# Performance work log

Hardware: AMD Instinct MI355X
Metric: run time of the kernel (lower is better)

Reference implementation:

```python
import jax, jax.numpy as jnp
import numpy as np

CONF_THRES = 0.6   # non_max_suppression default
IOU_THRES = 0.45   # non_max_suppression default
MAX_WH = 4096.0    # class-offset trick constant
MAX_DET = 300
NC = 80


def xywh2xyxy(b):
    xy, wh = b[:, :2], b[:, 2:4]
    return jnp.concatenate([xy - wh / 2, xy + wh / 2], axis=1)


def box_iou(a, b):
    # a: [N,4], b: [M,4] xyxy -> [N,M]
    area_a = (a[:, 2] - a[:, 0]) * (a[:, 3] - a[:, 1])
    area_b = (b[:, 2] - b[:, 0]) * (b[:, 3] - b[:, 1])
    lt = jnp.maximum(a[:, None, :2], b[None, :, :2])
    rb = jnp.minimum(a[:, None, 2:], b[None, :, 2:])
    wh = jnp.clip(rb - lt, 0.0)
    inter = wh[..., 0] * wh[..., 1]
    return inter / (area_a[:, None] + area_b[None, :] - inter + 1e-9)


def nms_image(x):
    # x: [N, 85] = [xywh, obj, 80 class logits]
    N = x.shape[0]
    logits = x[:, 5:]
    obj = x[:, 4]
    cls = logits * obj[:, None]          # x[:,5:] *= x[:,4:5]
    box = xywh2xyxy(x[:, :4])
    conf = cls.max(axis=1)
    j = jnp.argmax(cls, axis=1)
    valid = (obj > CONF_THRES) & (conf > CONF_THRES)
    scores = jnp.where(valid, conf, -1.0)  # invalid sort last, never suppress
    boxes_off = box + (j.astype(x.dtype) * MAX_WH)[:, None]  # class offset NMS

    order = jnp.argsort(-scores)
    iou = box_iou(boxes_off[order], boxes_off[order])  # [N,N]
    idxs = jnp.arange(N)

    def body(i, keep):
        sup = (iou[i] > IOU_THRES) & (idxs > i) & keep[i]
        return keep & ~sup

    keep = jax.lax.fori_loop(0, N, body, valid[order])

    # rows = [xyxy, conf, cls_idx, 80 logits] in score-sorted order
    rows = jnp.concatenate([
        box[order],
        conf[order][:, None],
        j[order].astype(x.dtype)[:, None],
        logits[order],
    ], axis=1)  # [N, 86]

    rank = jnp.cumsum(keep) - 1
    dest = jnp.where(keep & (rank < MAX_DET), rank, MAX_DET)  # dropped -> slot MAX_DET
    out = jnp.zeros((MAX_DET + 1, rows.shape[1]), x.dtype).at[dest].set(rows)
    return out[:MAX_DET]  # [300, 86]; zero rows = no detection


def setup_inputs() -> dict:
    key = jax.random.key(0)
    score = jax.random.normal(key, (32, 425, 17, 17), dtype=jnp.float32)
    return {"score": score}


def reference(score):
    B, C, H, W = score.shape
    # view(B, 425, H*W).transpose(1,2).view(B, H*W*5, 85)
    pred = score.reshape(B, C, H * W)
    pred = jnp.transpose(pred, (0, 2, 1)).reshape(B, H * W * 5, 85)
    return jax.vmap(nms_image)(pred)  # [B, 300, 86] = [xyxy, conf, cls, 80 logits]
```

## Files before the change

### kernel.cpp

```cpp
#include <hip/hip_runtime.h>

#define NPRED 1445
#define RAWSTR 1472
#define NCLS  80
#define MAXDET 300
#define OUTC  86
#define CONF_T 0.6f
#define IOU_T  0.45f
#define MAX_WH 4096.0f
#define HWSZ  289
#define NIMG  32
#define SLOTS 768
#define MCAP  512
#define EPB   256
#define EWALK 2048

#define OFF_CNT  128
#define OFF_KEYR 256
#define OFF_BOXR 377088
#define OFF_KEY  1130752
#define OFF_SBOX 1327360
#define OFF_ECNT 1720576
#define OFF_EDG  1721600
#define OFF_DST  1983744
#define WS_NEED  2022144

__device__ __forceinline__ unsigned long long bcast64(unsigned long long v, int srcLane) {
    unsigned lo = (unsigned)__builtin_amdgcn_readlane((int)(unsigned)(v & 0xFFFFFFFFULL), srcLane);
    unsigned hi = (unsigned)__builtin_amdgcn_readlane((int)(unsigned)(v >> 32), srcLane);
    return ((unsigned long long)hi << 32) | lo;
}

__global__ __launch_bounds__(128)
void prep_kernel(const float* __restrict__ score, unsigned long long* __restrict__ wsKeyRaw,
                 float4* __restrict__ wsBoxRaw) {
    const int b = blockIdx.x;
    const int ci = blockIdx.y * 128 + threadIdx.x;
    if (ci >= NPRED) return;
    const int t5 = ci / HWSZ;
    const int hw = ci - t5 * HWSZ;
    const int n = hw * 5 + t5;
    const float* base = score + (size_t)b * 425 * HWSZ + (size_t)(t5 * 85) * HWSZ + hw;
    float x = base[0];
    float y = base[HWSZ];
    float w = base[2 * HWSZ];
    float h = base[3 * HWSZ];
    float obj = base[4 * HWSZ];

    float best = -INFINITY; int bj = 0;
    #pragma unroll 16
    for (int k = 0; k < NCLS; ++k) {
        float v = base[(5 + k) * HWSZ] * obj;
        if (v > best) { best = v; bj = k; }
    }

    float wh2 = w * 0.5f, hh2 = h * 0.5f;
    float x1 = x - wh2, y1 = y - hh2, x2 = x + wh2, y2 = y + hh2;
    float off = (float)bj * MAX_WH;

    unsigned long long key = ~0ULL;
    if ((obj > CONF_T) && (best > CONF_T)) {
        unsigned int u = __float_as_uint(best);
        unsigned int desc = ~(u | 0x80000000u);
        key = ((unsigned long long)desc << 32)
            | ((unsigned long long)(unsigned)n << 16)
            | ((unsigned long long)(unsigned)bj << 8);
    }
    wsKeyRaw[b * RAWSTR + ci] = key;
    wsBoxRaw[b * RAWSTR + ci] = make_float4(x1 + off, y1 + off, x2 + off, y2 + off);
}

struct EdgeSh {
    unsigned long long keys[NPRED];
    unsigned long long cke[SLOTS];
    unsigned short cidx[SLOTS];
    float sx1[SLOTS], sy1[SLOTS], sx2[SLOTS], sy2[SLOTS];
    int wtot[16];
    int mTot, ecnt;
};

__global__ __launch_bounds__(1024)
void edge_kernel(const unsigned long long* __restrict__ wsKeyRaw,
                 const float4* __restrict__ wsBoxRaw,
                 int* __restrict__ wsCnt, unsigned long long* __restrict__ wsKey,
                 float4* __restrict__ wsSBox,
                 int* __restrict__ wsECnt, unsigned int* __restrict__ wsEdges) {
    __shared__ EdgeSh s;
    const int b = blockIdx.x, w = blockIdx.y, tid = threadIdx.x;
    const int lane = tid & 63, wid = tid >> 6;

    for (int i = tid; i < NPRED; i += 1024) s.keys[i] = wsKeyRaw[b * RAWSTR + i];
    if (tid == 0) s.ecnt = 0;
    __syncthreads();

    const int i0 = tid, i1 = tid + 1024;
    const bool v0 = (s.keys[i0] >> 63) == 0ULL;
    const bool v1 = (i1 < NPRED) && ((s.keys[i1] >> 63) == 0ULL);
    int cnt = (int)v0 + (int)v1;
    int inc = cnt;
    #pragma unroll
    for (int m = 1; m < 64; m <<= 1) {
        int v = __shfl_up(inc, m, 64);
        if (lane >= m) inc += v;
    }
    if (lane == 63) s.wtot[wid] = inc;
    __syncthreads();
    int basep = 0;
    for (int w2 = 0; w2 < wid; ++w2) basep += s.wtot[w2];
    int pos = basep + inc - cnt;
    if (v0 && pos < SLOTS) s.cidx[pos] = (unsigned short)i0;
    if (v1 && pos + (int)v0 < SLOTS) s.cidx[pos + (int)v0] = (unsigned short)i1;
    if (tid == 0) {
        int t = 0;
        for (int w2 = 0; w2 < 16; ++w2) t += s.wtot[w2];
        s.mTot = t;
    }
    __syncthreads();
    int M = s.mTot; if (M > SLOTS) M = SLOTS;
    if (tid < M) s.cke[tid] = s.keys[s.cidx[tid]];
    __syncthreads();

    if (tid < M) {
        unsigned long long ki = s.cke[tid];
        int rank = 0;
        #pragma unroll 4
        for (int j2 = 0; j2 < M; ++j2) rank += (s.cke[j2] < ki) ? 1 : 0;
        float4 bx = wsBoxRaw[b * RAWSTR + s.cidx[tid]];
        s.sx1[rank] = bx.x; s.sy1[rank] = bx.y; s.sx2[rank] = bx.z; s.sy2[rank] = bx.w;
        if (w == 0) {
            wsKey[b * SLOTS + rank] = ki;
            wsSBox[b * SLOTS + rank] = bx;
        }
    }
    if (w == 0 && tid == 0) wsCnt[b] = M;
    __syncthreads();

    if (M > MCAP) { if (tid == 0) wsECnt[b * 8 + w] = 0x7FFFFFFF; return; }

    unsigned int* reg = wsEdges + (size_t)(b * 8 + w) * EPB;
    const int j = (w << 6) + lane;
    float jx1 = 0.f, jy1 = 0.f, jx2 = 0.f, jy2 = 0.f, ab = 0.f;
    const bool jok = (j < M);
    if (jok) {
        jx1 = s.sx1[j]; jy1 = s.sy1[j]; jx2 = s.sx2[j]; jy2 = s.sy2[j];
        ab = (jx2 - jx1) * (jy2 - jy1);
    }
    int ilim = (w + 1) << 6; if (ilim > M) ilim = M;
    for (int i = wid; i < ilim; i += 16) {
        float ax1 = s.sx1[i], ay1 = s.sy1[i], ax2 = s.sx2[i], ay2 = s.sy2[i];
        float aa = (ax2 - ax1) * (ay2 - ay1);
        bool sup = false;
        if (jok && j > i) {
            float ltx = fmaxf(ax1, jx1), lty = fmaxf(ay1, jy1);
            float rbx = fminf(ax2, jx2), rby = fminf(ay2, jy2);
            float ww = fmaxf(rbx - ltx, 0.0f), hh = fmaxf(rby - lty, 0.0f);
            float inter = ww * hh;
            float denom = ((aa + ab) - inter) + 1e-9f;
            sup = (inter / denom) > IOU_T;
        }
        unsigned long long mask = __ballot(sup);
        if (lane == 0 && mask) {
            int pc = __popcll(mask);
            int eb = atomicAdd(&s.ecnt, pc);
            int k = 0;
            while (mask) {
                int bit = __ffsll((long long)mask) - 1;
                mask &= mask - 1;
                int p = eb + k;
                if (p < EPB) reg[p] = ((unsigned)i << 9) | (unsigned)((w << 6) + bit);
                ++k;
            }
        }
    }
    __syncthreads();
    if (tid == 0) wsECnt[b * 8 + w] = s.ecnt;
}

struct ScanSh {
    union {
        struct {
            float x1[SLOTS], y1[SLOTS], x2[SLOTS], y2[SLOTS];
            unsigned char kp[SLOTS];
        } fb;
        struct { unsigned int eraw[EWALK]; unsigned int esrt[EWALK]; } e;
    } u;
    int ec[8];
    int eoff[9];
    int over;
};

__global__ __launch_bounds__(256)
void scan_kernel(const int* __restrict__ wsCnt, const int* __restrict__ wsECnt,
                 const unsigned int* __restrict__ wsEdges, const float4* __restrict__ wsSBox,
                 int* __restrict__ wsKept, int* __restrict__ wsDst) {
    __shared__ ScanSh sh;
    const int b = blockIdx.x, tid = threadIdx.x, lane = tid & 63;
    int M = wsCnt[b]; if (M > SLOTS) M = SLOTS;
    if (tid < 8) sh.ec[tid] = wsECnt[b * 8 + tid];
    if (tid == 0) sh.over = 0;
    __syncthreads();
    if (tid == 0) {
        int o = 0;
        for (int w = 0; w < 8; ++w) {
            sh.eoff[w] = o;
            int c = sh.ec[w];
            if (c > EPB) { sh.over = 1; c = EPB; }
            o += c;
        }
        sh.eoff[8] = o;
    }
    __syncthreads();
    const bool fast = (M <= MCAP) && (sh.over == 0);
    const int Etot = sh.eoff[8];

    if (fast) {
        for (int w = 0; w < 8; ++w) {
            int c = sh.ec[w]; if (c > EPB) c = EPB;
            const unsigned int* reg = wsEdges + (size_t)(b * 8 + w) * EPB;
            for (int e2 = tid; e2 < c; e2 += 256) sh.u.e.eraw[sh.eoff[w] + e2] = reg[e2];
        }
        __syncthreads();
        for (int e2 = tid; e2 < Etot; e2 += 256) {
            unsigned int ke = sh.u.e.eraw[e2];
            int rank = 0;
            for (int j2 = 0; j2 < Etot; ++j2) rank += (sh.u.e.eraw[j2] < ke) ? 1 : 0;
            sh.u.e.esrt[rank] = ke;
        }
        __syncthreads();
        if (tid >= 64) return;
        unsigned long long Kw = 0ULL;
        { int rem = M - (lane << 6);
          if (rem >= 64) Kw = ~0ULL; else if (rem > 0) Kw = (~0ULL) >> (64 - rem); }
        unsigned int A[8], B[8];
#define LOADE(buf, bs) { _Pragma("unroll") for (int k = 0; k < 8; ++k) { \
        int e2 = (bs) + k; buf[k] = (e2 < Etot) ? sh.u.e.esrt[e2] : 0xFFFFFFFFu; } }
#define PROCE(buf) { _Pragma("unroll") for (int k = 0; k < 8; ++k) { \
        unsigned int ek = buf[k]; \
        if (ek != 0xFFFFFFFFu) { \
            int ei = (int)(ek >> 9), ej = (int)(ek & 511u); \
            unsigned long long kwi = bcast64(Kw, ei >> 6); \
            if ((kwi >> (ei & 63)) & 1ULL) { \
                if (lane == (ej >> 6)) Kw &= ~(1ULL << (ej & 63)); \
            } } } }
        LOADE(A, 0)
        for (int e = 0; e < Etot; e += 16) {
            LOADE(B, e + 8)
            PROCE(A)
            LOADE(A, e + 16)
            PROCE(B)
        }
#undef LOADE
#undef PROCE
        int myc = __popcll(Kw);
        int incc = myc;
        #pragma unroll
        for (int m = 1; m < 64; m <<= 1) {
            int v = __shfl_up(incc, m, 64);
            if (lane >= m) incc += v;
        }
        int tot = __shfl(incc, 63, 64);
        if (lane == 0) wsKept[b] = (tot < MAXDET) ? tot : MAXDET;
        int r = incc - myc;
        unsigned long long kw = Kw;
        while (kw) {
            int i = __ffsll((long long)kw) - 1;
            kw &= kw - 1;
            if (r < MAXDET) wsDst[b * MAXDET + r] = (lane << 6) + i;
            ++r;
        }
    } else {
        for (int r = tid; r < M; r += 256) {
            float4 v = wsSBox[b * SLOTS + r];
            sh.u.fb.x1[r] = v.x; sh.u.fb.y1[r] = v.y;
            sh.u.fb.x2[r] = v.z; sh.u.fb.y2[r] = v.w; sh.u.fb.kp[r] = 1;
        }
        __syncthreads();
        for (int i = 0; i < M; ++i) {
            if (sh.u.fb.kp[i]) {
                float ax1 = sh.u.fb.x1[i], ay1 = sh.u.fb.y1[i];
                float ax2 = sh.u.fb.x2[i], ay2 = sh.u.fb.y2[i];
                float aa = (ax2 - ax1) * (ay2 - ay1);
                for (int r = i + 1 + tid; r < M; r += 256) {
                    float bx1 = sh.u.fb.x1[r], by1 = sh.u.fb.y1[r];
                    float bx2 = sh.u.fb.x2[r], by2 = sh.u.fb.y2[r];
                    float ab = (bx2 - bx1) * (by2 - by1);
                    float ltx = fmaxf(ax1, bx1), lty = fmaxf(ay1, by1);
                    float rbx = fminf(ax2, bx2), rby = fminf(ay2, by2);
                    float ww = fmaxf(rbx - ltx, 0.0f), hh = fmaxf(rby - lty, 0.0f);
                    float inter = ww * hh;
                    float denom = ((aa + ab) - inter) + 1e-9f;
                    if ((inter / denom) > IOU_T) sh.u.fb.kp[r] = 0;
                }
            }
            __syncthreads();
        }
        if (tid == 0) {
            int c2 = 0;
            for (int r = 0; r < M && c2 < MAXDET; ++r)
                if (sh.u.fb.kp[r]) wsDst[b * MAXDET + c2++] = r;
            wsKept[b] = c2;
        }
    }
}

__global__ __launch_bounds__(256)
void out_kernel(const float* __restrict__ score, const int* __restrict__ wsKept,
                const unsigned long long* __restrict__ wsKey,
                const int* __restrict__ wsDst, float* __restrict__ out) {
    const int b = blockIdx.x;
    const int e = blockIdx.y * 256 + threadIdx.x;
    if (e >= MAXDET * OUTC) return;
    const int row = e / OUTC, c = e - row * OUTC;
    float v = 0.0f;
    if (row < wsKept[b]) {
        unsigned long long key = wsKey[b * SLOTS + wsDst[b * MAXDET + row]];
        int n = (int)((key >> 16) & 0xFFFFULL);
        int cls = (int)((key >> 8) & 0xFFULL);
        int hw = n / 5, t5 = n - hw * 5;
        const float* base = score + (size_t)b * 425 * HWSZ + (size_t)(t5 * 85) * HWSZ + hw;
        if (c < 4) {
            float x = base[0];
            float y = base[HWSZ];
            float w = base[2 * HWSZ];
            float h = base[3 * HWSZ];
            float wh2 = w * 0.5f, hh2 = h * 0.5f;
            v = (c == 0) ? (x - wh2) : (c == 1) ? (y - hh2)
              : (c == 2) ? (x + wh2) : (y + hh2);
        } else if (c == 4) {
            v = __uint_as_float((~(unsigned int)(key >> 32)) & 0x7FFFFFFFu);
        } else if (c == 5) {
            v = (float)cls;
        } else {
            v = base[(c - 1) * HWSZ];
        }
    }
    out[(size_t)b * MAXDET * OUTC + e] = v;
}

struct SMemFB {
    float bx1[NPRED], by1[NPRED], bx2[NPRED], by2[NPRED], area[NPRED];
    unsigned short sortedN[NPRED];
    union {
        unsigned long long vkey[NPRED];
        struct { float confR[MAXDET]; unsigned char jclsR[MAXDET]; } oi;
        unsigned char keepFB[NPRED];
    } u;
    unsigned short dstN[MAXDET];
    int validCount;
    int keptCount;
};

__device__ __forceinline__ void conf_argmax(const float* __restrict__ base, float obj,
                                            float& conf, int& bj) {
    float best = -INFINITY; int bjj = 0;
    #pragma unroll 8
    for (int k = 0; k < NCLS; ++k) {
        float v = base[(5 + k) * HWSZ] * obj;
        if (v > best) { best = v; bjj = k; }
    }
    conf = best; bj = bjj;
}

__global__ __launch_bounds__(1024)
void yolo_nms_single(const float* __restrict__ score, float* __restrict__ out) {
    __shared__ SMemFB s;
    const int b = blockIdx.x;
    const int tid = threadIdx.x;
    const float* sb = score + (size_t)b * 425 * HWSZ;
    if (tid == 0) s.validCount = 0;
    __syncthreads();
    for (int ci = tid; ci < NPRED; ci += 1024) {
        int t5 = ci / HWSZ;
        int hw = ci - t5 * HWSZ;
        int n = hw * 5 + t5;
        const float* base = sb + (size_t)(t5 * 85) * HWSZ + hw;
        float x = base[0], y = base[HWSZ], w = base[2 * HWSZ], h = base[3 * HWSZ];
        float obj = base[4 * HWSZ];
        float conf; int bj;
        conf_argmax(base, obj, conf, bj);
        bool valid = (obj > CONF_T) && (conf > CONF_T);
        float wh2 = w * 0.5f, hh2 = h * 0.5f;
        float x1 = x - wh2, y1 = y - hh2, x2 = x + wh2, y2 = y + hh2;
        float off = (float)bj * MAX_WH;
        float ox1 = x1 + off, oy1 = y1 + off, ox2 = x2 + off, oy2 = y2 + off;
        s.bx1[n] = ox1; s.by1[n] = oy1; s.bx2[n] = ox2; s.by2[n] = oy2;
        s.area[n] = (ox2 - ox1) * (oy2 - oy1);
        if (valid) {
            int slot = atomicAdd(&s.validCount, 1);
            unsigned int uu = __float_as_uint(conf);
            unsigned int desc = ~(uu | 0x80000000u);
            s.u.vkey[slot] = ((unsigned long long)desc << 32) | (unsigned int)n;
        }
    }
    __syncthreads();
    const int M = s.validCount;
    for (int vi = tid; vi < M; vi += 1024) {
        unsigned long long ki = s.u.vkey[vi];
        int rank = 0;
        for (int j = 0; j < M; ++j) rank += (s.u.vkey[j] < ki) ? 1 : 0;
        s.sortedN[rank] = (unsigned short)(ki & 0xFFFFULL);
    }
    __syncthreads();
    for (int r = tid; r < M; r += 1024) s.u.keepFB[r] = 1;
    __syncthreads();
    for (int i = 0; i < M; ++i) {
        if (s.u.keepFB[i]) {
            int ni = s.sortedN[i];
            float ax1 = s.bx1[ni], ay1 = s.by1[ni], ax2 = s.bx2[ni], ay2 = s.by2[ni];
            float aa = s.area[ni];
            for (int r = i + 1 + tid; r < M; r += 1024) {
                int nj = s.sortedN[r];
                float ltx = fmaxf(ax1, s.bx1[nj]);
                float lty = fmaxf(ay1, s.by1[nj]);
                float rbx = fminf(ax2, s.bx2[nj]);
                float rby = fminf(ay2, s.by2[nj]);
                float ww = fmaxf(rbx - ltx, 0.0f);
                float hh = fmaxf(rby - lty, 0.0f);
                float inter = ww * hh;
                float denom = ((aa + s.area[nj]) - inter) + 1e-9f;
                if ((inter / denom) > IOU_T) s.u.keepFB[r] = 0;
            }
        }
        __syncthreads();
    }
    if (tid == 0) {
        int cnt = 0;
        for (int r = 0; r < M && cnt < MAXDET; ++r)
            if (s.u.keepFB[r]) s.dstN[cnt++] = s.sortedN[r];
        s.keptCount = cnt;
    }
    __syncthreads();
    const int cnt = s.keptCount;
    if (tid < cnt) {
        int n = s.dstN[tid];
        int hw = n / 5, t5 = n - hw * 5;
        const float* base = sb + (size_t)(t5 * 85) * HWSZ + hw;
        float obj = base[4 * HWSZ];
        float conf; int bj;
        conf_argmax(base, obj, conf, bj);
        s.u.oi.confR[tid] = conf;
        s.u.oi.jclsR[tid] = (unsigned char)bj;
    }
    __syncthreads();
    float* ob = out + (size_t)b * MAXDET * OUTC;
    for (int e = tid; e < MAXDET * OUTC; e += 1024) {
        int row = e / OUTC, c = e - row * OUTC;
        float v = 0.0f;
        if (row < cnt) {
            int n = s.dstN[row];
            int hw = n / 5, t5 = n - hw * 5;
            const float* base = sb + (size_t)(t5 * 85) * HWSZ + hw;
            if (c < 4) {
                float x = base[0], y = base[HWSZ], w = base[2 * HWSZ], h = base[3 * HWSZ];
                float wh2 = w * 0.5f, hh2 = h * 0.5f;
                v = (c == 0) ? (x - wh2) : (c == 1) ? (y - hh2)
                  : (c == 2) ? (x + wh2) : (y + hh2);
            } else if (c == 4) {
                v = s.u.oi.confR[row];
            } else if (c == 5) {
                v = (float)s.u.oi.jclsR[row];
            } else {
                v = base[(c - 1) * HWSZ];
            }
        }
        ob[e] = v;
    }
}

extern "C" void kernel_launch(void* const* d_in, const int* in_sizes, int n_in,
                              void* d_out, int out_size, void* d_ws, size_t ws_size,
                              hipStream_t stream) {
    const float* score = (const float*)d_in[0];
    float* out = (float*)d_out;
    char* ws = (char*)d_ws;
    int* wsKept = (int*)ws;
    int* wsCnt  = (int*)(ws + OFF_CNT);
    unsigned long long* wsKeyRaw = (unsigned long long*)(ws + OFF_KEYR);
    float4* wsBoxRaw = (float4*)(ws + OFF_BOXR);
    unsigned long long* wsKey = (unsigned long long*)(ws + OFF_KEY);
    float4* wsSBox = (float4*)(ws + OFF_SBOX);
    int* wsECnt = (int*)(ws + OFF_ECNT);
    unsigned int* wsEdges = (unsigned int*)(ws + OFF_EDG);
    int* wsDst = (int*)(ws + OFF_DST);

    if (ws_size >= (size_t)WS_NEED) {
        prep_kernel<<<dim3(NIMG, 12), 128, 0, stream>>>(score, wsKeyRaw, wsBoxRaw);
        edge_kernel<<<dim3(NIMG, 8), 1024, 0, stream>>>(wsKeyRaw, wsBoxRaw, wsCnt,
                                                        wsKey, wsSBox, wsECnt, wsEdges);
        scan_kernel<<<NIMG, 256, 0, stream>>>(wsCnt, wsECnt, wsEdges, wsSBox, wsKept, wsDst);
        out_kernel<<<dim3(NIMG, 101), 256, 0, stream>>>(score, wsKept, wsKey, wsDst, out);
    } else {
        yolo_nms_single<<<NIMG, 1024, 0, stream>>>(score, out);
    }
}
```

Measured before the change: 42.69 us.

## Fuse NMS scan into output kernel, recomputing keep set per block

Merges the per-image suppression scan and the output scatter into one kernel launched over (image, 101) blocks. Each block redundantly sorts the edge list and walks it to rebuild the keep set in shared memory, then writes its own slice of output rows. This removes one kernel launch and the global round trip for kept counts and destination indices. In exchange the sort and walk are repeated 101 times per image, and a sentinel-count tweak is added to the overflow handling.

```diff
diff --git a/kernel.cpp b/kernel.cpp
--- a/kernel.cpp
+++ b/kernel.cpp
@@ -176,24 +176,28 @@
     if (tid == 0) wsECnt[b * 8 + w] = s.ecnt;
 }
 
-struct ScanSh {
+struct OutSh {
     union {
+        struct { unsigned int eraw[EWALK]; unsigned int esrt[EWALK]; } e;
         struct {
             float x1[SLOTS], y1[SLOTS], x2[SLOTS], y2[SLOTS];
             unsigned char kp[SLOTS];
         } fb;
-        struct { unsigned int eraw[EWALK]; unsigned int esrt[EWALK]; } e;
     } u;
     int ec[8];
     int eoff[9];
     int over;
+    unsigned short dstR[MAXDET];
+    int keptTot;
 };
 
 __global__ __launch_bounds__(256)
-void scan_kernel(const int* __restrict__ wsCnt, const int* __restrict__ wsECnt,
-                 const unsigned int* __restrict__ wsEdges, const float4* __restrict__ wsSBox,
-                 int* __restrict__ wsKept, int* __restrict__ wsDst) {
-    __shared__ ScanSh sh;
+void out_nms_kernel(const float* __restrict__ score, const int* __restrict__ wsCnt,
+                    const int* __restrict__ wsECnt, const unsigned int* __restrict__ wsEdges,
+                    const float4* __restrict__ wsSBox,
+                    const unsigned long long* __restrict__ wsKey,
+                    float* __restrict__ out) {
+    __shared__ OutSh sh;
     const int b = blockIdx.x, tid = threadIdx.x, lane = tid & 63;
     int M = wsCnt[b]; if (M > SLOTS) M = SLOTS;
     if (tid < 8) sh.ec[tid] = wsECnt[b * 8 + tid];
@@ -204,7 +208,7 @@
         for (int w = 0; w < 8; ++w) {
             sh.eoff[w] = o;
             int c = sh.ec[w];
-            if (c > EPB) { sh.over = 1; c = EPB; }
+            if (c > EPB) { sh.over = 1; c = (c == 0x7FFFFFFF) ? 0 : EPB; }
             o += c;
         }
         sh.eoff[8] = o;
@@ -227,47 +231,49 @@
             sh.u.e.esrt[rank] = ke;
         }
         __syncthreads();
-        if (tid >= 64) return;
-        unsigned long long Kw = 0ULL;
-        { int rem = M - (lane << 6);
-          if (rem >= 64) Kw = ~0ULL; else if (rem > 0) Kw = (~0ULL) >> (64 - rem); }
-        unsigned int A[8], B[8];
+        if (tid < 64) {
+            unsigned long long Kw = 0ULL;
+            { int rem = M - (lane << 6);
+              if (rem >= 64) Kw = ~0ULL; else if (rem > 0) Kw = (~0ULL) >> (64 - rem); }
+            unsigned int A[8], B[8];
 #define LOADE(buf, bs) { _Pragma("unroll") for (int k = 0; k < 8; ++k) { \
-        int e2 = (bs) + k; buf[k] = (e2 < Etot) ? sh.u.e.esrt[e2] : 0xFFFFFFFFu; } }
+            int e2 = (bs) + k; buf[k] = (e2 < Etot) ? sh.u.e.esrt[e2] : 0xFFFFFFFFu; } }
 #define PROCE(buf) { _Pragma("unroll") for (int k = 0; k < 8; ++k) { \
-        unsigned int ek = buf[k]; \
-        if (ek != 0xFFFFFFFFu) { \
-            int ei = (int)(ek >> 9), ej = (int)(ek & 511u); \
-            unsigned long long kwi = bcast64(Kw, ei >> 6); \
-            if ((kwi >> (ei & 63)) & 1ULL) { \
-                if (lane == (ej >> 6)) Kw &= ~(1ULL << (ej & 63)); \
-            } } } }
-        LOADE(A, 0)
-        for (int e = 0; e < Etot; e += 16) {
-            LOADE(B, e + 8)
-            PROCE(A)
-            LOADE(A, e + 16)
-            PROCE(B)
-        }
+            unsigned int ek = buf[k]; \
+            if (ek != 0xFFFFFFFFu) { \
+                int ei = (int)(ek >> 9), ej = (int)(ek & 511u); \
+                unsigned long long kwi = bcast64(Kw, ei >> 6); \
+                if ((kwi >> (ei & 63)) & 1ULL) { \
+                    if (lane == (ej >> 6)) Kw &= ~(1ULL << (ej & 63)); \
+                } } } }
+            LOADE(A, 0)
+            for (int e = 0; e < Etot; e += 16) {
+                LOADE(B, e + 8)
+                PROCE(A)
+                LOADE(A, e + 16)
+                PROCE(B)
+            }
 #undef LOADE
 #undef PROCE
-        int myc = __popcll(Kw);
-        int incc = myc;
-        #pragma unroll
-        for (int m = 1; m < 64; m <<= 1) {
-            int v = __shfl_up(incc, m, 64);
-            if (lane >= m) incc += v;
-        }
-        int tot = __shfl(incc, 63, 64);
-        if (lane == 0) wsKept[b] = (tot < MAXDET) ? tot : MAXDET;
-        int r = incc - myc;
-        unsigned long long kw = Kw;
-        while (kw) {
-            int i = __ffsll((long long)kw) - 1;
-            kw &= kw - 1;
-            if (r < MAXDET) wsDst[b * MAXDET + r] = (lane << 6) + i;
-            ++r;
-        }
+            int myc = __popcll(Kw);
+            int incc = myc;
+            #pragma unroll
+            for (int m = 1; m < 64; m <<= 1) {
+                int v = __shfl_up(incc, m, 64);
+                if (lane >= m) incc += v;
+            }
+            int tot = __shfl(incc, 63, 64);
+            if (lane == 0) sh.keptTot = (tot < MAXDET) ? tot : MAXDET;
+            int r = incc - myc;
+            unsigned long long kw = Kw;
+            while (kw) {
+                int i = __ffsll((long long)kw) - 1;
+                kw &= kw - 1;
+                if (r < MAXDET) sh.dstR[r] = (unsigned short)((lane << 6) + i);
+                ++r;
+            }
+        }
+        __syncthreads();
     } else {
         for (int r = tid; r < M; r += 256) {
             float4 v = wsSBox[b * SLOTS + r];
@@ -297,23 +303,19 @@
         if (tid == 0) {
             int c2 = 0;
             for (int r = 0; r < M && c2 < MAXDET; ++r)
-                if (sh.u.fb.kp[r]) wsDst[b * MAXDET + c2++] = r;
-            wsKept[b] = c2;
-        }
-    }
-}
-
-__global__ __launch_bounds__(256)
-void out_kernel(const float* __restrict__ score, const int* __restrict__ wsKept,
-                const unsigned long long* __restrict__ wsKey,
-                const int* __restrict__ wsDst, float* __restrict__ out) {
-    const int b = blockIdx.x;
-    const int e = blockIdx.y * 256 + threadIdx.x;
+                if (sh.u.fb.kp[r]) sh.dstR[c2++] = (unsigned short)r;
+            sh.keptTot = c2;
+        }
+        __syncthreads();
+    }
+
+    const int cnt = sh.keptTot;
+    const int e = blockIdx.y * 256 + tid;
     if (e >= MAXDET * OUTC) return;
     const int row = e / OUTC, c = e - row * OUTC;
     float v = 0.0f;
-    if (row < wsKept[b]) {
-        unsigned long long key = wsKey[b * SLOTS + wsDst[b * MAXDET + row]];
+    if (row < cnt) {
+        unsigned long long key = wsKey[b * SLOTS + sh.dstR[row]];
         int n = (int)((key >> 16) & 0xFFFFULL);
         int cls = (int)((key >> 8) & 0xFFULL);
         int hw = n / 5, t5 = n - hw * 5;
@@ -473,7 +475,6 @@
     const float* score = (const float*)d_in[0];
     float* out = (float*)d_out;
     char* ws = (char*)d_ws;
-    int* wsKept = (int*)ws;
     int* wsCnt  = (int*)(ws + OFF_CNT);
     unsigned long long* wsKeyRaw = (unsigned long long*)(ws + OFF_KEYR);
     float4* wsBoxRaw = (float4*)(ws + OFF_BOXR);
@@ -481,14 +482,13 @@
     float4* wsSBox = (float4*)(ws + OFF_SBOX);
     int* wsECnt = (int*)(ws + OFF_ECNT);
     unsigned int* wsEdges = (unsigned int*)(ws + OFF_EDG);
-    int* wsDst = (int*)(ws + OFF_DST);
 
     if (ws_size >= (size_t)WS_NEED) {
         prep_kernel<<<dim3(NIMG, 12), 128, 0, stream>>>(score, wsKeyRaw, wsBoxRaw);
         edge_kernel<<<dim3(NIMG, 8), 1024, 0, stream>>>(wsKeyRaw, wsBoxRaw, wsCnt,
                                                         wsKey, wsSBox, wsECnt, wsEdges);
-        scan_kernel<<<NIMG, 256, 0, stream>>>(wsCnt, wsECnt, wsEdges, wsSBox, wsKept, wsDst);
-        out_kernel<<<dim3(NIMG, 101), 256, 0, stream>>>(score, wsKept, wsKey, wsDst, out);
+        out_nms_kernel<<<dim3(NIMG, 101), 256, 0, stream>>>(score, wsCnt, wsECnt, wsEdges,
+                                                            wsSBox, wsKey, out);
     } else {
         yolo_nms_single<<<NIMG, 1024, 0, stream>>>(score, out);
     }
```

Result: slower. 48.08 us (+12.6%).
